# Kernel tuning notes

Measured on AMD Instinct MI355X. Metric: run time of the kernel, lower is better.

## Reference

```python
import jax, jax.numpy as jnp
import numpy as np

WS = 7          # window_size
SHIFT = 3       # shift_size
HEADS = 3
DIM = 96
HID = 384       # mlp_ratio * dim
EPS = 1e-5


def _rel_pos_index(ws):
    coords = np.stack(np.meshgrid(np.arange(ws), np.arange(ws), indexing='ij')).reshape(2, -1)
    rel = (coords[:, :, None] - coords[:, None, :]).transpose(1, 2, 0)
    rel[:, :, 0] += ws - 1
    rel[:, :, 1] += ws - 1
    rel[:, :, 0] *= 2 * ws - 1
    return jnp.asarray(rel.sum(-1))  # (ws*ws, ws*ws) int

REL_IDX = _rel_pos_index(WS)


def _shift_mask(H, W):
    # standard Swin SW-MSA mask: (nW, N, N), 0 / -100
    img = np.zeros((H, W), dtype=np.int32)
    cnt = 0
    for h in (slice(0, -WS), slice(-WS, -SHIFT), slice(-SHIFT, None)):
        for w in (slice(0, -WS), slice(-WS, -SHIFT), slice(-SHIFT, None)):
            img[h, w] = cnt
            cnt += 1
    win = img.reshape(H // WS, WS, W // WS, WS).transpose(0, 2, 1, 3).reshape(-1, WS * WS)
    diff = win[:, None, :] - win[:, :, None]
    return jnp.asarray(np.where(diff != 0, -100.0, 0.0).astype(np.float32))


def _ln(x, g, b):
    m = x.mean(-1, keepdims=True)
    v = ((x - m) ** 2).mean(-1, keepdims=True)
    return (x - m) * jax.lax.rsqrt(v + EPS) * g + b


def setup_inputs() -> dict:
    key = jax.random.key(0)
    ks = jax.random.split(key, 12)
    B, H, W, C = 16, 112, 112, DIM
    s = 0.02
    return {
        'x': jax.random.normal(ks[0], (B, H * W, C), jnp.float32),
        'mask': _shift_mask(H, W),
        'norm1_g': jnp.ones((C,), jnp.float32),
        'norm1_b': jnp.zeros((C,), jnp.float32),
        'qkv_w': jax.random.normal(ks[1], (3 * C, C), jnp.float32) * s,
        'qkv_b': jnp.zeros((3 * C,), jnp.float32),
        'rel_bias_table': jax.random.normal(ks[2], ((2 * WS - 1) ** 2, HEADS), jnp.float32) * s,
        'proj_w': jax.random.normal(ks[3], (C, C), jnp.float32) * s,
        'proj_b': jnp.zeros((C,), jnp.float32),
        'norm2_g': jnp.ones((C,), jnp.float32),
        'norm2_b': jnp.zeros((C,), jnp.float32),
        'fc1_w': jax.random.normal(ks[4], (HID, C), jnp.float32) * s,
        'fc1_b': jnp.zeros((HID,), jnp.float32),
        'fc2_w': jax.random.normal(ks[5], (C, HID), jnp.float32) * s,
        'fc2_b': jnp.zeros((C,), jnp.float32),
        'H': 112,
        'W': 112,
    }


def reference(x, mask, norm1_g, norm1_b, qkv_w, qkv_b, rel_bias_table, proj_w,
              proj_b, norm2_g, norm2_b, fc1_w, fc1_b, fc2_w, fc2_b, H, W):
    B, L, C = x.shape
    N = WS * WS
    hd = C // HEADS
    scale = hd ** -0.5
    nh, nw = H // WS, W // WS

    shortcut = x
    h = _ln(x, norm1_g, norm1_b).reshape(B, H, W, C)
    # cyclic shift
    h = jnp.roll(h, (-SHIFT, -SHIFT), axis=(1, 2))
    # window partition -> (B*nW, N, C)
    xw = h.reshape(B, nh, WS, nw, WS, C).transpose(0, 1, 3, 2, 4, 5).reshape(-1, N, C)
    B_ = xw.shape[0]

    qkv = (xw @ qkv_w.T + qkv_b).reshape(B_, N, 3, HEADS, hd).transpose(2, 0, 3, 1, 4)
    q, k, v = qkv[0], qkv[1], qkv[2]          # (B_, heads, N, hd)
    attn = jnp.einsum('bhnd,bhmd->bhnm', q * scale, k)

    bias = rel_bias_table[REL_IDX.reshape(-1)].reshape(N, N, HEADS).transpose(2, 0, 1)
    attn = attn + bias[None]

    nW = mask.shape[0]
    attn = attn.reshape(B_ // nW, nW, HEADS, N, N) + mask[None, :, None]
    attn = jax.nn.softmax(attn.reshape(B_, HEADS, N, N), axis=-1)

    out = jnp.einsum('bhnm,bhmd->bhnd', attn, v).transpose(0, 2, 1, 3).reshape(B_, N, C)
    out = out @ proj_w.T + proj_b

    # window reverse + reverse shift
    out = out.reshape(B, nh, nw, WS, WS, C).transpose(0, 1, 3, 2, 4, 5).reshape(B, H, W, C)
    out = jnp.roll(out, (SHIFT, SHIFT), axis=(1, 2)).reshape(B, L, C)

    x = shortcut + out
    y = _ln(x, norm2_g, norm2_b)
    y = jax.nn.gelu(y @ fc1_w.T + fc1_b, approximate=False)
    y = y @ fc2_w.T + fc2_b
    return x + y
```

## Files before the change

kernel.cpp:

```cpp
#include <hip/hip_runtime.h>
#include <hip/hip_bf16.h>
#include <math.h>


typedef __attribute__((ext_vector_type(8))) short bfrag8;
typedef __attribute__((ext_vector_type(4))) float f32x4;

__device__ __forceinline__ float bf2f(unsigned short u){
  union { unsigned int i; float f; } c; c.i = ((unsigned int)u) << 16; return c.f;
}
__device__ __forceinline__ unsigned short f2bf(float f){
  __hip_bfloat16 h = __float2bfloat16(f);
  union { __hip_bfloat16 h; unsigned short u; } c; c.h = h; return c.u;
}
__device__ __forceinline__ float gelu_f(float x){
  float x2 = x * x;
  float z  = x + 0.044715f * x * x2;
  float u  = __expf(-1.5957691f * z);
  return x / (1.f + u);
}

__device__ __forceinline__ int swz32(int r, int c){
  return r * 32 + (c ^ (((r ^ (r >> 2)) & 3) << 3));
}
__device__ __forceinline__ int swz64(int r, int c){
  return r * 64 + (c ^ (((r ^ (r >> 3)) & 7) << 3));
}
__device__ __forceinline__ int fswz(int r, int c){
  return r * 96 + (c ^ ((r & 7) << 2));
}

__device__ __forceinline__ int win_to_img(int r){
  int win = r / 49, n = r - win * 49;
  int b  = win >> 8, wi = win & 255;
  int wh = wi >> 4,  ww = wi & 15;
  int i  = n / 7,    j  = n - i * 7;
  int hs = wh * 7 + i + 3; if (hs >= 112) hs -= 112;
  int ws = ww * 7 + j + 3; if (ws >= 112) ws -= 112;
  return b * 12544 + hs * 112 + ws;
}

__global__ __launch_bounds__(256) void cvt_all_kernel(
    const float* __restrict__ s1, unsigned short* __restrict__ d1,
    const float* __restrict__ s2, unsigned short* __restrict__ d2,
    const float* __restrict__ s3, unsigned short* __restrict__ d3,
    const float* __restrict__ s4, unsigned short* __restrict__ d4)
{
  int i = blockIdx.x * 256 + threadIdx.x;
  if      (i < 36864)  d1[i]          = f2bf(s1[i]);
  else if (i < 73728)  d2[i - 36864]  = f2bf(s2[i - 36864]);
  else if (i < 101376) d3[i - 73728]  = f2bf(s3[i - 73728]);
  else if (i < 110592) d4[i - 101376] = f2bf(s4[i - 101376]);
}

__global__ __launch_bounds__(256) void cb_kernel(
    const float* __restrict__ relt, const float* __restrict__ mask,
    float* __restrict__ cbt)
{
  int idx = blockIdx.x * 256 + threadIdx.x;
  int wh = idx >> 12;
  int w = wh / 3, h = wh - w * 3;
  int rem = idx & 4095;
  int mt = rem >> 10, nt = (rem >> 8) & 3, qd = (rem >> 6) & 3;
  int ln = (rem >> 2) & 15, r = rem & 3;
  int m = mt * 16 + qd * 4 + r, n = nt * 16 + ln;
  float v;
  if (m < 49 && n < 49){
    int i1 = m / 7, j1 = m - i1 * 7;
    int i2 = n / 7, j2 = n - i2 * 7;
    int ridx = (i1 - i2 + 6) * 13 + (j1 - j2 + 6);
    v = relt[ridx * 3 + h] + mask[w * 2401 + m * 49 + n];
  } else if (n >= 49) v = -10000.0f;
  else v = 0.0f;
  cbt[idx] = v;
}

__global__ __launch_bounds__(256, 4) void fused_win_kernel(
    const float* __restrict__ x,
    const float* __restrict__ g1, const float* __restrict__ b1n,
    const unsigned short* __restrict__ wqkv, const float* __restrict__ bqkv,
    const float* __restrict__ cbt,
    const unsigned short* __restrict__ wproj, const float* __restrict__ bproj,
    unsigned short* __restrict__ x2)
{
  __shared__ unsigned short L[18944];

  int win = blockIdx.x, tid = threadIdx.x;
  const float scale = 0.17677669529663687f;

  {
    int r = tid >> 2, part = tid & 3;
    if (r < 49){
      int gr = win_to_img(win * 49 + r);
      const float* rowp = x + (size_t)gr * 96 + part * 24;
      float v[24]; float s = 0.f, q = 0.f;
      #pragma unroll
      for (int c = 0; c < 24; c++){ v[c] = rowp[c]; s += v[c]; q += v[c] * v[c]; }
      s += __shfl_xor(s, 1); q += __shfl_xor(q, 1);
      s += __shfl_xor(s, 2); q += __shfl_xor(q, 2);
      float mean = s * (1.f / 96.f);
      float rs = rsqrtf(q * (1.f / 96.f) - mean * mean + 1e-5f);
      #pragma unroll
      for (int c = 0; c < 24; c++){
        int cc = part * 24 + c;
        L[r * 104 + cc] = f2bf((v[c] - mean) * rs * g1[cc] + b1n[cc]);
      }
    } else {
      #pragma unroll
      for (int c = 0; c < 24; c++) L[r * 104 + part * 24 + c] = 0;
    }
  }
  __syncthreads();

  int wave = tid >> 6, lane = tid & 63;
  int ln = lane & 15, qd = lane >> 4;

  bfrag8 af[4][3];
  #pragma unroll
  for (int mt = 0; mt < 4; mt++)
    #pragma unroll
    for (int k3 = 0; k3 < 3; k3++)
      af[mt][k3] = *reinterpret_cast<const bfrag8*>(
          &L[(mt * 16 + ln) * 104 + k3 * 32 + qd * 8]);
  __syncthreads();

  {
    int nct = (wave < 2) ? 5 : 4;
    for (int i = 0; i < nct; i++){
      int nt = wave + i * 4;
      int col = nt * 16 + ln;
      const unsigned short* wp = wqkv + (size_t)col * 96 + qd * 8;
      bfrag8 B0 = *reinterpret_cast<const bfrag8*>(wp);
      bfrag8 B1 = *reinterpret_cast<const bfrag8*>(wp + 32);
      bfrag8 B2 = *reinterpret_cast<const bfrag8*>(wp + 64);
      float bs = bqkv[col];
      #pragma unroll
      for (int mt = 0; mt < 4; mt++){
        f32x4 acc = {bs, bs, bs, bs};
        acc = __builtin_amdgcn_mfma_f32_16x16x32_bf16(af[mt][0], B0, acc, 0, 0, 0);
        acc = __builtin_amdgcn_mfma_f32_16x16x32_bf16(af[mt][1], B1, acc, 0, 0, 0);
        acc = __builtin_amdgcn_mfma_f32_16x16x32_bf16(af[mt][2], B2, acc, 0, 0, 0);
        if (nt < 6){
          int hh = col >> 5, d = col & 31;
          #pragma unroll
          for (int r = 0; r < 4; r++){
            int m = mt * 16 + qd * 4 + r;
            L[6656 + hh * 4096 + swz32(m, d)] = f2bf(acc[r] * scale);
          }
        } else if (nt < 12){
          int cc = col - 96; int hh = cc >> 5, d = cc & 31;
          #pragma unroll
          for (int r = 0; r < 4; r++){
            int m = mt * 16 + qd * 4 + r;
            L[6656 + hh * 4096 + 2048 + swz32(m, d)] = f2bf(acc[r]);
          }
        } else {
          int cc = col - 192; int hh = cc >> 5, d = cc & 31;
          #pragma unroll
          for (int r = 0; r < 4; r++){
            int m = mt * 16 + qd * 4 + r;
            L[hh * 2048 + swz64(d, m)] = f2bf(acc[r]);
          }
        }
      }
    }
  }
  __syncthreads();

  int h = wave;
  float invs[4][4];
  if (wave < 3){
    bfrag8 qf[4];
    #pragma unroll
    for (int mt = 0; mt < 4; mt++)
      qf[mt] = *reinterpret_cast<const bfrag8*>(
          &L[6656 + h * 4096 + swz32(mt * 16 + ln, qd * 8)]);
    const float* cbh = cbt + ((size_t)(win & 255) * 3 + h) * 4096;
    f32x4 sf[4][4];
    #pragma unroll
    for (int nt = 0; nt < 4; nt++){
      bfrag8 kf = *reinterpret_cast<const bfrag8*>(
          &L[6656 + h * 4096 + 2048 + swz32(nt * 16 + ln, qd * 8)]);
      #pragma unroll
      for (int mt = 0; mt < 4; mt++){
        f32x4 cv = *reinterpret_cast<const f32x4*>(
            cbh + mt * 1024 + nt * 256 + qd * 64 + ln * 4);
        sf[mt][nt] = __builtin_amdgcn_mfma_f32_16x16x32_bf16(qf[mt], kf, cv, 0, 0, 0);
      }
    }
    #pragma unroll
    for (int mt = 0; mt < 4; mt++){
      float mx[4], sm[4];
      #pragma unroll
      for (int r = 0; r < 4; r++)
        mx[r] = fmaxf(fmaxf(sf[mt][0][r], sf[mt][1][r]),
                      fmaxf(sf[mt][2][r], sf[mt][3][r]));
      #pragma unroll
      for (int r = 0; r < 4; r++)
        #pragma unroll
        for (int off = 1; off < 16; off <<= 1)
          mx[r] = fmaxf(mx[r], __shfl_xor(mx[r], off));
      #pragma unroll
      for (int r = 0; r < 4; r++){
        float e0 = __expf(sf[mt][0][r] - mx[r]);
        float e1 = __expf(sf[mt][1][r] - mx[r]);
        float e2 = __expf(sf[mt][2][r] - mx[r]);
        float e3 = __expf(sf[mt][3][r] - mx[r]);
        sf[mt][0][r] = e0; sf[mt][1][r] = e1; sf[mt][2][r] = e2; sf[mt][3][r] = e3;
        sm[r] = e0 + e1 + e2 + e3;
      }
      #pragma unroll
      for (int r = 0; r < 4; r++)
        #pragma unroll
        for (int off = 1; off < 16; off <<= 1)
          sm[r] += __shfl_xor(sm[r], off);
      #pragma unroll
      for (int r = 0; r < 4; r++){
        invs[mt][r] = 1.f / sm[r];
        int m = mt * 16 + qd * 4 + r;
        #pragma unroll
        for (int nt = 0; nt < 4; nt++)
          L[6656 + h * 4096 + swz64(m, nt * 16 + ln)] = f2bf(sf[mt][nt][r]);
      }
    }

    f32x4 of[4][2];
    #pragma unroll
    for (int mt = 0; mt < 4; mt++)
      #pragma unroll
      for (int dt = 0; dt < 2; dt++) of[mt][dt] = (f32x4){0.f, 0.f, 0.f, 0.f};
    #pragma unroll
    for (int k2 = 0; k2 < 2; k2++){
      bfrag8 vf[2];
      #pragma unroll
      for (int dt = 0; dt < 2; dt++)
        vf[dt] = *reinterpret_cast<const bfrag8*>(
            &L[h * 2048 + swz64(dt * 16 + ln, k2 * 32 + qd * 8)]);
      #pragma unroll
      for (int mt = 0; mt < 4; mt++){
        bfrag8 pf = *reinterpret_cast<const bfrag8*>(
            &L[6656 + h * 4096 + swz64(mt * 16 + ln, k2 * 32 + qd * 8)]);
        #pragma unroll
        for (int dt = 0; dt < 2; dt++)
          of[mt][dt] = __builtin_amdgcn_mfma_f32_16x16x32_bf16(pf, vf[dt], of[mt][dt], 0, 0, 0);
      }
    }
    #pragma unroll
    for (int mt = 0; mt < 4; mt++)
      #pragma unroll
      for (int r = 0; r < 4; r++){
        int m = mt * 16 + qd * 4 + r;
        #pragma unroll
        for (int dt = 0; dt < 2; dt++)
          L[h * 2048 + swz32(m, dt * 16 + ln)] = f2bf(of[mt][dt][r] * invs[mt][r]);
      }
  }
  __syncthreads();

  {
    int rh = wave >> 1, nh = wave & 1;
    bfrag8 ap[2][3];
    #pragma unroll
    for (int mt2 = 0; mt2 < 2; mt2++)
      #pragma unroll
      for (int k3 = 0; k3 < 3; k3++)
        ap[mt2][k3] = *reinterpret_cast<const bfrag8*>(
            &L[k3 * 2048 + swz32(rh * 32 + mt2 * 16 + ln, qd * 8)]);
    float* Xf = reinterpret_cast<float*>(&L[6656]);
    #pragma unroll
    for (int nt3 = 0; nt3 < 3; nt3++){
      int col = (nh * 3 + nt3) * 16 + ln;
      const unsigned short* wp = wproj + (size_t)col * 96 + qd * 8;
      bfrag8 B0 = *reinterpret_cast<const bfrag8*>(wp);
      bfrag8 B1 = *reinterpret_cast<const bfrag8*>(wp + 32);
      bfrag8 B2 = *reinterpret_cast<const bfrag8*>(wp + 64);
      float bv = bproj[col];
      #pragma unroll
      for (int mt2 = 0; mt2 < 2; mt2++){
        f32x4 acc = {bv, bv, bv, bv};
        acc = __builtin_amdgcn_mfma_f32_16x16x32_bf16(ap[mt2][0], B0, acc, 0, 0, 0);
        acc = __builtin_amdgcn_mfma_f32_16x16x32_bf16(ap[mt2][1], B1, acc, 0, 0, 0);
        acc = __builtin_amdgcn_mfma_f32_16x16x32_bf16(ap[mt2][2], B2, acc, 0, 0, 0);
        #pragma unroll
        for (int r = 0; r < 4; r++)
          Xf[fswz(rh * 32 + mt2 * 16 + qd * 4 + r, col)] = acc[r];
      }
    }
  }
  __syncthreads();

  {
    int r = tid >> 2, part = tid & 3;
    if (r < 49){
      int gi = win_to_img(win * 49 + r);
      const float* Xf = reinterpret_cast<const float*>(&L[6656]);
      const float* rowp = x + (size_t)gi * 96 + part * 24;
      int sxm = (r & 7) << 2;
      unsigned short ov[24];
      #pragma unroll
      for (int t6 = 0; t6 < 6; t6++){
        int cc = part * 24 + t6 * 4;
        f32x4 pv = *reinterpret_cast<const f32x4*>(&Xf[r * 96 + (cc ^ sxm)]);
        f32x4 rv = *reinterpret_cast<const f32x4*>(&rowp[t6 * 4]);
        #pragma unroll
        for (int j = 0; j < 4; j++)
          ov[t6 * 4 + j] = f2bf(pv[j] + rv[j]);
      }
      unsigned short* dst = x2 + (size_t)gi * 96 + part * 24;
      #pragma unroll
      for (int t3 = 0; t3 < 3; t3++)
        *reinterpret_cast<bfrag8*>(dst + t3 * 8) =
            *reinterpret_cast<const bfrag8*>(&ov[t3 * 8]);
    }
  }
}

__global__ __launch_bounds__(384, 4) void mlp_mfma_kernel(
    const unsigned short* __restrict__ x2,
    const float* __restrict__ g, const float* __restrict__ b,
    const unsigned short* __restrict__ w1, const float* __restrict__ b1,
    const unsigned short* __restrict__ w2, const float* __restrict__ b2,
    float* __restrict__ out)
{
  __shared__ unsigned short S[25088];
  unsigned short* As = S;
  unsigned short* Hs = S;
  int tid = threadIdx.x;
  int row0 = blockIdx.x * 64;

  {
    int r = tid / 6, c = (tid - r * 6) * 16;
    *reinterpret_cast<bfrag8*>(&As[r * 104 + c]) =
        *reinterpret_cast<const bfrag8*>(x2 + (size_t)(row0 + r) * 96 + c);
    *reinterpret_cast<bfrag8*>(&As[r * 104 + c + 8]) =
        *reinterpret_cast<const bfrag8*>(x2 + (size_t)(row0 + r) * 96 + c + 8);
  }
  __syncthreads();
  if (tid < 256){
    int rr = tid >> 2, part = tid & 3;
    float v[24]; float s = 0.f, q = 0.f;
    #pragma unroll
    for (int c = 0; c < 24; c++){
      v[c] = bf2f(As[rr * 104 + part * 24 + c]);
      s += v[c]; q += v[c] * v[c];
    }
    s += __shfl_xor(s, 1); q += __shfl_xor(q, 1);
    s += __shfl_xor(s, 2); q += __shfl_xor(q, 2);
    float mean = s * (1.f / 96.f);
    float rs = rsqrtf(q * (1.f / 96.f) - mean * mean + 1e-5f);
    #pragma unroll
    for (int c = 0; c < 24; c++){
      int cc = part * 24 + c;
      As[rr * 104 + cc] = f2bf((v[c] - mean) * rs * g[cc] + b[cc]);
    }
  }
  __syncthreads();

  int wave = tid / 64, lane = tid & 63;
  int ln = lane & 15, qd = lane >> 4;

  bfrag8 af[4][3];
  #pragma unroll
  for (int mt = 0; mt < 4; mt++)
    #pragma unroll
    for (int k3 = 0; k3 < 3; k3++)
      af[mt][k3] = *reinterpret_cast<const bfrag8*>(
          &As[(mt * 16 + ln) * 104 + k3 * 32 + qd * 8]);
  __syncthreads();

  for (int i = 0; i < 4; i++){
    int ntl = wave + i * 6;
    int col = ntl * 16 + ln;
    const unsigned short* wp = w1 + (size_t)col * 96 + qd * 8;
    bfrag8 B0 = *reinterpret_cast<const bfrag8*>(wp);
    bfrag8 B1 = *reinterpret_cast<const bfrag8*>(wp + 32);
    bfrag8 B2 = *reinterpret_cast<const bfrag8*>(wp + 64);
    float bias = b1[col];
    #pragma unroll
    for (int mt = 0; mt < 4; mt++){
      f32x4 a = {bias, bias, bias, bias};
      a = __builtin_amdgcn_mfma_f32_16x16x32_bf16(af[mt][0], B0, a, 0, 0, 0);
      a = __builtin_amdgcn_mfma_f32_16x16x32_bf16(af[mt][1], B1, a, 0, 0, 0);
      a = __builtin_amdgcn_mfma_f32_16x16x32_bf16(af[mt][2], B2, a, 0, 0, 0);
      #pragma unroll
      for (int r = 0; r < 4; r++)
        Hs[(mt * 16 + qd * 4 + r) * 392 + col] = f2bf(gelu_f(a[r]));
    }
  }
  __syncthreads();

  int col = wave * 16 + ln;
  float bias = b2[col];
  f32x4 acc[4];
  #pragma unroll
  for (int mt = 0; mt < 4; mt++) acc[mt] = (f32x4){bias, bias, bias, bias};
  for (int k2 = 0; k2 < 12; k2++){
    bfrag8 B = *reinterpret_cast<const bfrag8*>(
        w2 + (size_t)(wave * 16 + ln) * 384 + k2 * 32 + qd * 8);
    #pragma unroll
    for (int mt = 0; mt < 4; mt++){
      bfrag8 p = *reinterpret_cast<const bfrag8*>(
          &Hs[(mt * 16 + ln) * 392 + k2 * 32 + qd * 8]);
      acc[mt] = __builtin_amdgcn_mfma_f32_16x16x32_bf16(p, B, acc[mt], 0, 0, 0);
    }
  }
  {
    #pragma unroll
    for (int mt = 0; mt < 4; mt++)
      #pragma unroll
      for (int r = 0; r < 4; r++){
        int grow = row0 + mt * 16 + qd * 4 + r;
        out[(size_t)grow * 96 + col] =
            acc[mt][r] + bf2f(x2[(size_t)grow * 96 + col]);
      }
  }
}

extern "C" void kernel_launch(void* const* d_in, const int* in_sizes, int n_in,
                              void* d_out, int out_size, void* d_ws, size_t ws_size,
                              hipStream_t stream)
{
  const float* x      = (const float*)d_in[0];
  const float* mask   = (const float*)d_in[1];
  const float* n1g    = (const float*)d_in[2];
  const float* n1b    = (const float*)d_in[3];
  const float* qkv_w  = (const float*)d_in[4];
  const float* qkv_b  = (const float*)d_in[5];
  const float* relt   = (const float*)d_in[6];
  const float* proj_w = (const float*)d_in[7];
  const float* proj_b = (const float*)d_in[8];
  const float* n2g    = (const float*)d_in[9];
  const float* n2b    = (const float*)d_in[10];
  const float* fc1_w  = (const float*)d_in[11];
  const float* fc1_b  = (const float*)d_in[12];
  const float* fc2_w  = (const float*)d_in[13];
  const float* fc2_b  = (const float*)d_in[14];
  float* outp = (float*)d_out;
  (void)in_sizes; (void)n_in; (void)out_size; (void)ws_size; (void)mask;

  const size_t M = 200704;
  char* ws = (char*)d_ws;
  unsigned short* x2     = (unsigned short*)ws;
  size_t o = M * 96 * 2;
  unsigned short* w1bf   = (unsigned short*)(ws + o); o += 384 * 96 * 2;
  unsigned short* w2bf   = (unsigned short*)(ws + o); o += 96 * 384 * 2;
  unsigned short* wqkvbf = (unsigned short*)(ws + o); o += 288 * 96 * 2;
  unsigned short* wprojbf= (unsigned short*)(ws + o); o += 96 * 96 * 2;
  float*          cbuf   = (float*)(ws + o); o += (size_t)256 * 3 * 4096 * 4;

  cvt_all_kernel<<<432, 256, 0, stream>>>(
      fc1_w, w1bf, fc2_w, w2bf, qkv_w, wqkvbf, proj_w, wprojbf);
  cb_kernel<<<12288, 256, 0, stream>>>(relt, mask, cbuf);
  fused_win_kernel<<<4096, 256, 0, stream>>>(
      x, n1g, n1b, wqkvbf, qkv_b, cbuf, wprojbf, proj_b, x2);
  mlp_mfma_kernel<<<1568 * 2, 384, 0, stream>>>(
      x2, n2g, n2b, w1bf, fc1_b, w2bf, fc2_b, outp);
}
```

Baseline: 337.0 us.

## Fold scales into weights, use exp2 softmax, and vectorize LDS stores via swapped MFMA operands

The attention scale and log2(e) are pre-multiplied into the Q weights, Q bias and the bias/mask table, so softmax uses exp2 and a hardware reciprocal with normalization applied before the PV matmul. MFMA operands are swapped so each lane holds four contiguous output columns, which turns scalar bf16 LDS stores into packed 8-byte stores for Q/K, attention output and the MLP hidden layer. GELU is rewritten as exp2 plus rcp, and LayerNorm writes become 16-byte vector stores; the MLP kernel now reads x2 straight from global memory instead of staging it through LDS with an extra barrier. Using an approximate reciprocal and bf16 rounding of probabilities before normalization may change numerics slightly.

```diff
diff --git a/kernel.cpp b/kernel.cpp
--- a/kernel.cpp
+++ b/kernel.cpp
@@ -5,6 +5,9 @@
 
 typedef __attribute__((ext_vector_type(8))) short bfrag8;
 typedef __attribute__((ext_vector_type(4))) float f32x4;
+typedef __attribute__((ext_vector_type(2))) unsigned int u32x2;
+
+#define LOG2E 1.4426950408889634f
 
 __device__ __forceinline__ float bf2f(unsigned short u){
   union { unsigned int i; float f; } c; c.i = ((unsigned int)u) << 16; return c.f;
@@ -13,11 +16,18 @@
   __hip_bfloat16 h = __float2bfloat16(f);
   union { __hip_bfloat16 h; unsigned short u; } c; c.h = h; return c.u;
 }
+__device__ __forceinline__ u32x2 pack4(float a0, float a1, float a2, float a3){
+  u32x2 r;
+  r.x = (unsigned int)f2bf(a0) | ((unsigned int)f2bf(a1) << 16);
+  r.y = (unsigned int)f2bf(a2) | ((unsigned int)f2bf(a3) << 16);
+  return r;
+}
 __device__ __forceinline__ float gelu_f(float x){
+  const float c1 = -2.302208198f, c2 = -0.1029432397f;
   float x2 = x * x;
-  float z  = x + 0.044715f * x * x2;
-  float u  = __expf(-1.5957691f * z);
-  return x / (1.f + u);
+  float t  = __builtin_fmaf(x2, c2, c1);
+  float u  = exp2f(x * t);
+  return x * __builtin_amdgcn_rcpf(1.f + u);
 }
 
 __device__ __forceinline__ int swz32(int r, int c){
@@ -44,13 +54,26 @@
     const float* __restrict__ s1, unsigned short* __restrict__ d1,
     const float* __restrict__ s2, unsigned short* __restrict__ d2,
     const float* __restrict__ s3, unsigned short* __restrict__ d3,
-    const float* __restrict__ s4, unsigned short* __restrict__ d4)
+    const float* __restrict__ s4, unsigned short* __restrict__ d4,
+    const float* __restrict__ bq, float* __restrict__ bqs)
 {
+  const float QS = 0.17677669529663687f * 1.4426950408889634f;
   int i = blockIdx.x * 256 + threadIdx.x;
   if      (i < 36864)  d1[i]          = f2bf(s1[i]);
   else if (i < 73728)  d2[i - 36864]  = f2bf(s2[i - 36864]);
-  else if (i < 101376) d3[i - 73728]  = f2bf(s3[i - 73728]);
+  else if (i < 101376){
+    int j = i - 73728;
+    float v = s3[j];
+    if (j < 9216) v *= QS;
+    d3[j] = f2bf(v);
+  }
   else if (i < 110592) d4[i - 101376] = f2bf(s4[i - 101376]);
+  else if (i < 110880){
+    int j = i - 110592;
+    float v = bq[j];
+    if (j < 96) v *= QS;
+    bqs[j] = v;
+  }
 }
 
 __global__ __launch_bounds__(256) void cb_kernel(
@@ -69,7 +92,7 @@
     int i1 = m / 7, j1 = m - i1 * 7;
     int i2 = n / 7, j2 = n - i2 * 7;
     int ridx = (i1 - i2 + 6) * 13 + (j1 - j2 + 6);
-    v = relt[ridx * 3 + h] + mask[w * 2401 + m * 49 + n];
+    v = (relt[ridx * 3 + h] + mask[w * 2401 + m * 49 + n]) * LOG2E;
   } else if (n >= 49) v = -10000.0f;
   else v = 0.0f;
   cbt[idx] = v;
@@ -78,7 +101,7 @@
 __global__ __launch_bounds__(256, 4) void fused_win_kernel(
     const float* __restrict__ x,
     const float* __restrict__ g1, const float* __restrict__ b1n,
-    const unsigned short* __restrict__ wqkv, const float* __restrict__ bqkv,
+    const unsigned short* __restrict__ wqkv, const float* __restrict__ bqs,
     const float* __restrict__ cbt,
     const unsigned short* __restrict__ wproj, const float* __restrict__ bproj,
     unsigned short* __restrict__ x2)
@@ -86,7 +109,6 @@
   __shared__ unsigned short L[18944];
 
   int win = blockIdx.x, tid = threadIdx.x;
-  const float scale = 0.17677669529663687f;
 
   {
     int r = tid >> 2, part = tid & 3;
@@ -100,14 +122,21 @@
       s += __shfl_xor(s, 2); q += __shfl_xor(q, 2);
       float mean = s * (1.f / 96.f);
       float rs = rsqrtf(q * (1.f / 96.f) - mean * mean + 1e-5f);
+      unsigned short ov[24];
       #pragma unroll
       for (int c = 0; c < 24; c++){
         int cc = part * 24 + c;
-        L[r * 104 + cc] = f2bf((v[c] - mean) * rs * g1[cc] + b1n[cc]);
-      }
+        ov[c] = f2bf((v[c] - mean) * rs * g1[cc] + b1n[cc]);
+      }
+      #pragma unroll
+      for (int t = 0; t < 3; t++)
+        *reinterpret_cast<bfrag8*>(&L[r * 104 + part * 24 + t * 8]) =
+            *reinterpret_cast<const bfrag8*>(&ov[t * 8]);
     } else {
-      #pragma unroll
-      for (int c = 0; c < 24; c++) L[r * 104 + part * 24 + c] = 0;
+      bfrag8 z = {0, 0, 0, 0, 0, 0, 0, 0};
+      #pragma unroll
+      for (int t = 0; t < 3; t++)
+        *reinterpret_cast<bfrag8*>(&L[r * 104 + part * 24 + t * 8]) = z;
     }
   }
   __syncthreads();
@@ -128,47 +157,45 @@
     int nct = (wave < 2) ? 5 : 4;
     for (int i = 0; i < nct; i++){
       int nt = wave + i * 4;
-      int col = nt * 16 + ln;
-      const unsigned short* wp = wqkv + (size_t)col * 96 + qd * 8;
+      int col0 = nt * 16;
+      const unsigned short* wp = wqkv + (size_t)(col0 + ln) * 96 + qd * 8;
       bfrag8 B0 = *reinterpret_cast<const bfrag8*>(wp);
       bfrag8 B1 = *reinterpret_cast<const bfrag8*>(wp + 32);
       bfrag8 B2 = *reinterpret_cast<const bfrag8*>(wp + 64);
-      float bs = bqkv[col];
-      #pragma unroll
-      for (int mt = 0; mt < 4; mt++){
-        f32x4 acc = {bs, bs, bs, bs};
-        acc = __builtin_amdgcn_mfma_f32_16x16x32_bf16(af[mt][0], B0, acc, 0, 0, 0);
-        acc = __builtin_amdgcn_mfma_f32_16x16x32_bf16(af[mt][1], B1, acc, 0, 0, 0);
-        acc = __builtin_amdgcn_mfma_f32_16x16x32_bf16(af[mt][2], B2, acc, 0, 0, 0);
-        if (nt < 6){
-          int hh = col >> 5, d = col & 31;
-          #pragma unroll
-          for (int r = 0; r < 4; r++){
-            int m = mt * 16 + qd * 4 + r;
-            L[6656 + hh * 4096 + swz32(m, d)] = f2bf(acc[r] * scale);
-          }
-        } else if (nt < 12){
-          int cc = col - 96; int hh = cc >> 5, d = cc & 31;
-          #pragma unroll
-          for (int r = 0; r < 4; r++){
-            int m = mt * 16 + qd * 4 + r;
-            L[6656 + hh * 4096 + 2048 + swz32(m, d)] = f2bf(acc[r]);
-          }
-        } else {
-          int cc = col - 192; int hh = cc >> 5, d = cc & 31;
-          #pragma unroll
-          for (int r = 0; r < 4; r++){
-            int m = mt * 16 + qd * 4 + r;
-            L[hh * 2048 + swz64(d, m)] = f2bf(acc[r]);
-          }
+      if (nt < 12){
+        f32x4 bs4 = *reinterpret_cast<const f32x4*>(bqs + col0 + qd * 4);
+        int c0 = (nt < 6) ? col0 : (col0 - 96);
+        int base = 6656 + (c0 >> 5) * 4096 + ((nt < 6) ? 0 : 2048);
+        int d0 = (c0 & 31) + qd * 4;
+        #pragma unroll
+        for (int mt = 0; mt < 4; mt++){
+          f32x4 acc = bs4;
+          acc = __builtin_amdgcn_mfma_f32_16x16x32_bf16(B0, af[mt][0], acc, 0, 0, 0);
+          acc = __builtin_amdgcn_mfma_f32_16x16x32_bf16(B1, af[mt][1], acc, 0, 0, 0);
+          acc = __builtin_amdgcn_mfma_f32_16x16x32_bf16(B2, af[mt][2], acc, 0, 0, 0);
+          int m = mt * 16 + ln;
+          *reinterpret_cast<u32x2*>(&L[base + swz32(m, d0)]) =
+              pack4(acc[0], acc[1], acc[2], acc[3]);
         }
+      } else {
+        int cc = col0 + ln - 192; int hh = cc >> 5, d = cc & 31;
+        float bs = bqs[col0 + ln];
+        #pragma unroll
+        for (int mt = 0; mt < 4; mt++){
+          f32x4 acc = {bs, bs, bs, bs};
+          acc = __builtin_amdgcn_mfma_f32_16x16x32_bf16(af[mt][0], B0, acc, 0, 0, 0);
+          acc = __builtin_amdgcn_mfma_f32_16x16x32_bf16(af[mt][1], B1, acc, 0, 0, 0);
+          acc = __builtin_amdgcn_mfma_f32_16x16x32_bf16(af[mt][2], B2, acc, 0, 0, 0);
+          int m0 = mt * 16 + qd * 4;
+          *reinterpret_cast<u32x2*>(&L[hh * 2048 + swz64(d, m0)]) =
+              pack4(acc[0], acc[1], acc[2], acc[3]);
+        }
       }
     }
   }
   __syncthreads();
 
   int h = wave;
-  float invs[4][4];
   if (wave < 3){
     bfrag8 qf[4];
     #pragma unroll
@@ -202,10 +229,10 @@
           mx[r] = fmaxf(mx[r], __shfl_xor(mx[r], off));
       #pragma unroll
       for (int r = 0; r < 4; r++){
-        float e0 = __expf(sf[mt][0][r] - mx[r]);
-        float e1 = __expf(sf[mt][1][r] - mx[r]);
-        float e2 = __expf(sf[mt][2][r] - mx[r]);
-        float e3 = __expf(sf[mt][3][r] - mx[r]);
+        float e0 = exp2f(sf[mt][0][r] - mx[r]);
+        float e1 = exp2f(sf[mt][1][r] - mx[r]);
+        float e2 = exp2f(sf[mt][2][r] - mx[r]);
+        float e3 = exp2f(sf[mt][3][r] - mx[r]);
         sf[mt][0][r] = e0; sf[mt][1][r] = e1; sf[mt][2][r] = e2; sf[mt][3][r] = e3;
         sm[r] = e0 + e1 + e2 + e3;
       }
@@ -216,11 +243,11 @@
           sm[r] += __shfl_xor(sm[r], off);
       #pragma unroll
       for (int r = 0; r < 4; r++){
-        invs[mt][r] = 1.f / sm[r];
+        float inv = __builtin_amdgcn_rcpf(sm[r]);
         int m = mt * 16 + qd * 4 + r;
         #pragma unroll
         for (int nt = 0; nt < 4; nt++)
-          L[6656 + h * 4096 + swz64(m, nt * 16 + ln)] = f2bf(sf[mt][nt][r]);
+          L[6656 + h * 4096 + swz64(m, nt * 16 + ln)] = f2bf(sf[mt][nt][r] * inv);
       }
     }
 
@@ -242,17 +269,16 @@
             &L[6656 + h * 4096 + swz64(mt * 16 + ln, k2 * 32 + qd * 8)]);
         #pragma unroll
         for (int dt = 0; dt < 2; dt++)
-          of[mt][dt] = __builtin_amdgcn_mfma_f32_16x16x32_bf16(pf, vf[dt], of[mt][dt], 0, 0, 0);
+          of[mt][dt] = __builtin_amdgcn_mfma_f32_16x16x32_bf16(vf[dt], pf, of[mt][dt], 0, 0, 0);
       }
     }
     #pragma unroll
     for (int mt = 0; mt < 4; mt++)
       #pragma unroll
-      for (int r = 0; r < 4; r++){
-        int m = mt * 16 + qd * 4 + r;
-        #pragma unroll
-        for (int dt = 0; dt < 2; dt++)
-          L[h * 2048 + swz32(m, dt * 16 + ln)] = f2bf(of[mt][dt][r] * invs[mt][r]);
+      for (int dt = 0; dt < 2; dt++){
+        int m = mt * 16 + ln, d0 = dt * 16 + qd * 4;
+        *reinterpret_cast<u32x2*>(&L[h * 2048 + swz32(m, d0)]) =
+            pack4(of[mt][dt][0], of[mt][dt][1], of[mt][dt][2], of[mt][dt][3]);
       }
   }
   __syncthreads();
@@ -328,31 +354,33 @@
   int tid = threadIdx.x;
   int row0 = blockIdx.x * 64;
 
-  {
-    int r = tid / 6, c = (tid - r * 6) * 16;
-    *reinterpret_cast<bfrag8*>(&As[r * 104 + c]) =
-        *reinterpret_cast<const bfrag8*>(x2 + (size_t)(row0 + r) * 96 + c);
-    *reinterpret_cast<bfrag8*>(&As[r * 104 + c + 8]) =
-        *reinterpret_cast<const bfrag8*>(x2 + (size_t)(row0 + r) * 96 + c + 8);
-  }
-  __syncthreads();
   if (tid < 256){
     int rr = tid >> 2, part = tid & 3;
+    const unsigned short* rp = x2 + (size_t)(row0 + rr) * 96 + part * 24;
     float v[24]; float s = 0.f, q = 0.f;
     #pragma unroll
-    for (int c = 0; c < 24; c++){
-      v[c] = bf2f(As[rr * 104 + part * 24 + c]);
-      s += v[c]; q += v[c] * v[c];
+    for (int t = 0; t < 3; t++){
+      bfrag8 w = *reinterpret_cast<const bfrag8*>(rp + t * 8);
+      #pragma unroll
+      for (int j = 0; j < 8; j++){
+        float f = bf2f((unsigned short)w[j]);
+        v[t * 8 + j] = f; s += f; q += f * f;
+      }
     }
     s += __shfl_xor(s, 1); q += __shfl_xor(q, 1);
     s += __shfl_xor(s, 2); q += __shfl_xor(q, 2);
     float mean = s * (1.f / 96.f);
     float rs = rsqrtf(q * (1.f / 96.f) - mean * mean + 1e-5f);
+    unsigned short ov[24];
     #pragma unroll
     for (int c = 0; c < 24; c++){
       int cc = part * 24 + c;
-      As[rr * 104 + cc] = f2bf((v[c] - mean) * rs * g[cc] + b[cc]);
-    }
+      ov[c] = f2bf((v[c] - mean) * rs * g[cc] + b[cc]);
+    }
+    #pragma unroll
+    for (int t = 0; t < 3; t++)
+      *reinterpret_cast<bfrag8*>(&As[rr * 104 + part * 24 + t * 8]) =
+          *reinterpret_cast<const bfrag8*>(&ov[t * 8]);
   }
   __syncthreads();
 
@@ -370,21 +398,21 @@
 
   for (int i = 0; i < 4; i++){
     int ntl = wave + i * 6;
-    int col = ntl * 16 + ln;
-    const unsigned short* wp = w1 + (size_t)col * 96 + qd * 8;
+    int col0 = ntl * 16;
+    const unsigned short* wp = w1 + (size_t)(col0 + ln) * 96 + qd * 8;
     bfrag8 B0 = *reinterpret_cast<const bfrag8*>(wp);
     bfrag8 B1 = *reinterpret_cast<const bfrag8*>(wp + 32);
     bfrag8 B2 = *reinterpret_cast<const bfrag8*>(wp + 64);
-    float bias = b1[col];
+    f32x4 bs4 = *reinterpret_cast<const f32x4*>(b1 + col0 + qd * 4);
     #pragma unroll
     for (int mt = 0; mt < 4; mt++){
-      f32x4 a = {bias, bias, bias, bias};
-      a = __builtin_amdgcn_mfma_f32_16x16x32_bf16(af[mt][0], B0, a, 0, 0, 0);
-      a = __builtin_amdgcn_mfma_f32_16x16x32_bf16(af[mt][1], B1, a, 0, 0, 0);
-      a = __builtin_amdgcn_mfma_f32_16x16x32_bf16(af[mt][2], B2, a, 0, 0, 0);
-      #pragma unroll
-      for (int r = 0; r < 4; r++)
-        Hs[(mt * 16 + qd * 4 + r) * 392 + col] = f2bf(gelu_f(a[r]));
+      f32x4 a = bs4;
+      a = __builtin_amdgcn_mfma_f32_16x16x32_bf16(B0, af[mt][0], a, 0, 0, 0);
+      a = __builtin_amdgcn_mfma_f32_16x16x32_bf16(B1, af[mt][1], a, 0, 0, 0);
+      a = __builtin_amdgcn_mfma_f32_16x16x32_bf16(B2, af[mt][2], a, 0, 0, 0);
+      int m = mt * 16 + ln;
+      *reinterpret_cast<u32x2*>(&Hs[m * 392 + col0 + qd * 4]) =
+          pack4(gelu_f(a[0]), gelu_f(a[1]), gelu_f(a[2]), gelu_f(a[3]));
     }
   }
   __syncthreads();
@@ -446,13 +474,14 @@
   unsigned short* w2bf   = (unsigned short*)(ws + o); o += 96 * 384 * 2;
   unsigned short* wqkvbf = (unsigned short*)(ws + o); o += 288 * 96 * 2;
   unsigned short* wprojbf= (unsigned short*)(ws + o); o += 96 * 96 * 2;
+  float*          bqs    = (float*)(ws + o);          o += 288 * 4 + 64;
   float*          cbuf   = (float*)(ws + o); o += (size_t)256 * 3 * 4096 * 4;
 
-  cvt_all_kernel<<<432, 256, 0, stream>>>(
-      fc1_w, w1bf, fc2_w, w2bf, qkv_w, wqkvbf, proj_w, wprojbf);
+  cvt_all_kernel<<<434, 256, 0, stream>>>(
+      fc1_w, w1bf, fc2_w, w2bf, qkv_w, wqkvbf, proj_w, wprojbf, qkv_b, bqs);
   cb_kernel<<<12288, 256, 0, stream>>>(relt, mask, cbuf);
   fused_win_kernel<<<4096, 256, 0, stream>>>(
-      x, n1g, n1b, wqkvbf, qkv_b, cbuf, wprojbf, proj_b, x2);
-  mlp_mfma_kernel<<<1568 * 2, 384, 0, stream>>>(
+      x, n1g, n1b, wqkvbf, bqs, cbuf, wprojbf, proj_b, x2);
+  mlp_mfma_kernel<<<3136, 384, 0, stream>>>(
       x2, n2g, n2b, w1bf, fc1_b, w2bf, fc2_b, outp);
 }
```

New measurement: 312.2 us. -7.3%, faster.
